# Optimization experiments

Measured on AMD Instinct MI355X. Metric: run time of the kernel, lower is better.

The kernel has to match this reference:

```python
import jax, jax.numpy as jnp
import numpy as np

C_M = 256   # norm_channel (msa channel)
C_Z = 128   # pair_channel
H = 8       # num_head
C = 32      # attention_channel per head


def layer_norm(x, gamma, beta, eps=1e-5):
    mu = jnp.mean(x, axis=-1, keepdims=True)
    var = jnp.var(x, axis=-1, keepdims=True)
    return (x - mu) * jax.lax.rsqrt(var + eps) * gamma + beta


def setup_inputs() -> dict:
    key = jax.random.key(0)
    ks = jax.random.split(key, 12)
    B, S, R = 1, 128, 256
    inp = {
        "msa_act": jax.random.normal(ks[0], (B, S, R, C_M), jnp.float32),
        "pair_act": jax.random.normal(ks[1], (B, R, R, C_Z), jnp.float32),
        "msa_mask": jnp.ones((B, S, R), jnp.float32),
        # query_norm params
        "qn_g": jnp.ones((C_M,), jnp.float32),
        "qn_b": jnp.zeros((C_M,), jnp.float32),
        # feat_2d_norm params
        "pn_g": jnp.ones((C_Z,), jnp.float32),
        "pn_b": jnp.zeros((C_Z,), jnp.float32),
        # feat_2d_weights: Linear(C_Z -> H, bias=False)
        "w2d": jax.random.normal(ks[2], (C_Z, H), jnp.float32) / np.sqrt(C_Z),
        # attention projections [C_M, H, C]
        "wq": jax.random.normal(ks[3], (C_M, H, C), jnp.float32) / np.sqrt(C_M),
        "wk": jax.random.normal(ks[4], (C_M, H, C), jnp.float32) / np.sqrt(C_M),
        "wv": jax.random.normal(ks[5], (C_M, H, C), jnp.float32) / np.sqrt(C_M),
        # gating linear [C_M, H, C] + bias
        "wg": jax.random.normal(ks[6], (C_M, H, C), jnp.float32) / np.sqrt(C_M),
        "bg": jnp.ones((H, C), jnp.float32),
        # output linear [H, C, C_M] + bias
        "wo": jax.random.normal(ks[7], (H, C, C_M), jnp.float32) / np.sqrt(H * C),
        "bo": jnp.zeros((C_M,), jnp.float32),
    }
    return inp


def reference(msa_act, pair_act, msa_mask, qn_g, qn_b, pn_g, pn_b, w2d,
              wq, wk, wv, wg, bg, wo, bo):
    # Pair bias: LayerNorm -> Linear(C_Z->H) -> permute to [B, 1, H, R, R]
    z = layer_norm(pair_act, pn_g, pn_b)            # [B, R, R, C_Z]
    z = jnp.einsum('bqkc,ch->bhqk', z, w2d)          # [B, H, R, R]
    z = z[:, None]                                   # [B, 1, H, R, R]

    # Mask bias: [B, S, 1, 1, R]
    mask_bias = (1e9 * (msa_mask - 1.0))[:, :, None, None, :]

    # Row-wise MHA with query norm
    m = layer_norm(msa_act, qn_g, qn_b)              # [B, S, R, C_M]
    scale = 1.0 / np.sqrt(C)
    q = jnp.einsum('bsqc,chd->bshqd', m, wq) * scale
    k = jnp.einsum('bskc,chd->bshkd', m, wk)
    v = jnp.einsum('bskc,chd->bshkd', m, wv)

    logits = jnp.einsum('bshqd,bshkd->bshqk', q, k) + mask_bias + z
    a = jax.nn.softmax(logits, axis=-1)              # [B, S, H, R, R]
    o = jnp.einsum('bshqk,bshkd->bsqhd', a, v)       # [B, S, R, H, C]

    g = jax.nn.sigmoid(jnp.einsum('bsqc,chd->bsqhd', m, wg) + bg)
    o = o * g
    out = jnp.einsum('bsqhd,hdc->bsqc', o, wo) + bo  # [B, S, R, C_M]
    return out
```

## Files before the change

### kernel.cpp

```cpp
#include <hip/hip_runtime.h>

typedef unsigned short u16;
typedef __attribute__((ext_vector_type(8))) short bf16x8;
typedef __attribute__((ext_vector_type(4))) float f32x4;

__device__ __forceinline__ float bf2f(u16 u){
  union { unsigned int i; float f; } v; v.i = ((unsigned int)u) << 16; return v.f;
}
__device__ __forceinline__ u16 f2bf(float f){
  union { float f; unsigned int i; } v; v.f = f;
  unsigned int i = v.i;
  return (u16)((i + 0x7fffu + ((i >> 16) & 1u)) >> 16);
}
__device__ __forceinline__ float ldin(const void* p, int i, int f){
  return f ? ((const float*)p)[i] : bf2f(((const u16*)p)[i]);
}
__device__ __forceinline__ bf16x8 pack8(const float* v){
  union { bf16x8 v8; u16 h[8]; } u;
  #pragma unroll
  for (int j = 0; j < 8; ++j) u.h[j] = f2bf(v[j]);
  return u.v8;
}
__device__ __forceinline__ void gload16(const u16* g, u16* l){
  __builtin_amdgcn_global_load_lds(
      (const __attribute__((address_space(1))) void*)g,
      (__attribute__((address_space(3))) void*)l, 16, 0, 0);
}

__global__ void k_sniff(const unsigned int* __restrict__ msa_w, int* __restrict__ flag)
{
  int lane = threadIdx.x & 63;
  int lo0 = 0, expok = 0;
  #pragma unroll
  for (int j = 0; j < 4; ++j) {
    unsigned int w = msa_w[lane * 4 + j];
    if ((w & 0xffffu) == 0u) lo0++;
    unsigned int e = (w >> 7) & 0xffu;
    if (e >= 110u && e <= 140u) expok++;
  }
  #pragma unroll
  for (int off = 1; off < 64; off <<= 1) {
    lo0   += __shfl_xor(lo0,   off, 64);
    expok += __shfl_xor(expok, off, 64);
  }
  if (lane == 0 && blockIdx.x == 0)
    *flag = (lo0 > 200) ? 1 : ((expok > 200) ? 0 : 1);
}

__global__ __launch_bounds__(256) void k_transpose(
    const void* __restrict__ wq, const void* __restrict__ wk,
    const void* __restrict__ wv, const void* __restrict__ wg,
    const void* __restrict__ wo, const int* __restrict__ flagp,
    u16* __restrict__ Wt, u16* __restrict__ wot)
{
  const int flag = *flagp;
  int idx = blockIdx.x * 256 + threadIdx.x;
  int mat = idx >> 16;
  int col = (idx >> 8) & 255;
  int c   = idx & 255;
  const void* src = (mat == 0) ? wq : (mat == 1) ? wk : (mat == 2) ? wv
                  : (mat == 3) ? wg : wo;
  u16 v = f2bf(ldin(src, c * 256 + col, flag));
  if (idx < 262144) Wt[idx] = v;
  else              wot[idx - 262144] = v;
}

__global__ __launch_bounds__(256) void k_pair_z(
    const void* __restrict__ pair, const void* __restrict__ png,
    const void* __restrict__ pnb, const void* __restrict__ w2d,
    const int* __restrict__ flagp, float* __restrict__ z)
{
  __shared__ u16 As[64 * 136];
  __shared__ u16 Bs[16 * 136];
  const int flag = *flagp;
  const int t = threadIdx.x, lane = t & 63, wave = t >> 6;
  const int g = lane >> 4, l15 = lane & 15;
  const int rowBase = blockIdx.x * 64;

  if (t < 128) {
    #pragma unroll
    for (int n = 0; n < 16; ++n)
      Bs[n * 136 + t] = (n < 8) ? f2bf(ldin(w2d, t * 8 + n, flag)) : (u16)0;
  }
  {
    int lrow = t >> 2, cb = (t & 3) * 32;
    int base = (rowBase + lrow) * 128 + cb;
    float x[32];
    if (flag) {
      const float* p = (const float*)pair + base;
      #pragma unroll
      for (int j = 0; j < 8; ++j) {
        float4 f4 = *(const float4*)(p + 4 * j);
        x[4*j] = f4.x; x[4*j+1] = f4.y; x[4*j+2] = f4.z; x[4*j+3] = f4.w;
      }
    } else {
      const u16* p = (const u16*)pair + base;
      #pragma unroll
      for (int j = 0; j < 4; ++j) {
        uint4 u = *(const uint4*)(p + 8 * j);
        const u16* h = (const u16*)&u;
        #pragma unroll
        for (int e = 0; e < 8; ++e) x[8*j+e] = bf2f(h[e]);
      }
    }
    float s = 0.f, sq = 0.f;
    #pragma unroll
    for (int j = 0; j < 32; ++j) { s += x[j]; sq += x[j] * x[j]; }
    s  += __shfl_xor(s, 1, 64);  s  += __shfl_xor(s, 2, 64);
    sq += __shfl_xor(sq, 1, 64); sq += __shfl_xor(sq, 2, 64);
    float mu = s * (1.f / 128.f);
    float var = sq * (1.f / 128.f) - mu * mu;
    float rs = rsqrtf(var + 1e-5f);
    u16 o[32];
    #pragma unroll
    for (int j = 0; j < 32; ++j) {
      int c = cb + j;
      o[j] = f2bf((x[j] - mu) * rs * ldin(png, c, flag) + ldin(pnb, c, flag));
    }
    u16* dst = As + lrow * 136 + cb;
    #pragma unroll
    for (int j = 0; j < 4; ++j)
      *(uint4*)(dst + 8 * j) = *(const uint4*)(o + 8 * j);
  }
  __syncthreads();

  f32x4 accz = {0.f, 0.f, 0.f, 0.f};
  #pragma unroll
  for (int kb = 0; kb < 4; ++kb) {
    bf16x8 a = *(const bf16x8*)(As + (wave * 16 + l15) * 136 + kb * 32 + g * 8);
    bf16x8 b = *(const bf16x8*)(Bs + l15 * 136 + kb * 32 + g * 8);
    accz = __builtin_amdgcn_mfma_f32_16x16x32_bf16(a, b, accz, 0, 0, 0);
  }
  if (l15 < 8) {
    #pragma unroll
    for (int r = 0; r < 4; ++r)
      z[l15 * 65536 + rowBase + wave * 16 + g * 4 + r] = accz[r];
  }
}

__global__ __launch_bounds__(256) void k_msa_ln(
    const void* __restrict__ msa, const void* __restrict__ qng,
    const void* __restrict__ qnb, const int* __restrict__ flagp,
    u16* __restrict__ m_bf)
{
  const int flag = *flagp;
  int wave = threadIdx.x >> 6, lane = threadIdx.x & 63;
  int row = blockIdx.x * 4 + wave;
  float x[4];
  if (flag) {
    float4 f4 = *((const float4*)msa + row * 64 + lane);
    x[0]=f4.x; x[1]=f4.y; x[2]=f4.z; x[3]=f4.w;
  } else {
    uint2 u = *((const uint2*)msa + row * 64 + lane);
    const u16* h = (const u16*)&u;
    #pragma unroll
    for (int j = 0; j < 4; ++j) x[j] = bf2f(h[j]);
  }
  float s = 0.f, sq = 0.f;
  #pragma unroll
  for (int j = 0; j < 4; ++j) { s += x[j]; sq += x[j] * x[j]; }
  #pragma unroll
  for (int off = 1; off < 64; off <<= 1) {
    s  += __shfl_xor(s,  off, 64);
    sq += __shfl_xor(sq, off, 64);
  }
  float mu = s * (1.f / 256.f);
  float var = sq * (1.f / 256.f) - mu * mu;
  float rs = rsqrtf(var + 1e-5f);
  u16 o[4];
  #pragma unroll
  for (int j = 0; j < 4; ++j) {
    int c = lane * 4 + j;
    o[j] = f2bf((x[j] - mu) * rs * ldin(qng, c, flag) + ldin(qnb, c, flag));
  }
  *((uint2*)m_bf + row * 64 + lane) = *(const uint2*)o;
}

__global__ __launch_bounds__(256) void k_qkvg(
    const u16* __restrict__ m_bf, const u16* __restrict__ Wt,
    const void* __restrict__ bg, const int* __restrict__ flagp,
    u16* __restrict__ q_ws, u16* __restrict__ k_ws,
    u16* __restrict__ v_ws, u16* __restrict__ g_ws)
{
  __shared__ u16 SM[64 * 136];
  u16* As = SM;
  u16* Bs = SM + 4096;
  const int flag = *flagp;
  const int t = threadIdx.x, lane = t & 63, wave = t >> 6;
  const int wm = (wave >> 1) * 64, wn = (wave & 1) * 64;
  const int rowBase = blockIdx.x * 128;
  const int colBase = blockIdx.y * 128;
  const int g = lane >> 4, l15 = lane & 15;
  const int srow = wave * 32 + (lane >> 2);
  const int scol = (lane & 3) * 8;
  const u16* gA = m_bf + (rowBase + srow) * 256 + scol;
  const u16* gB = Wt   + (colBase + srow) * 256 + scol;
  u16* lA = As + wave * 32 * 32;
  u16* lB = Bs + wave * 32 * 32;

  f32x4 acc[4][4];
  f32x4 zero = {0.f, 0.f, 0.f, 0.f};
  #pragma unroll
  for (int i = 0; i < 4; ++i)
    #pragma unroll
    for (int j = 0; j < 4; ++j) acc[i][j] = zero;

  for (int kb = 0; kb < 256; kb += 32) {
    __syncthreads();
    gload16(gA + kb,            lA);
    gload16(gA + kb + 16 * 256, lA + 16 * 32);
    gload16(gB + kb,            lB);
    gload16(gB + kb + 16 * 256, lB + 16 * 32);
    __syncthreads();
    bf16x8 a[4], b[4];
    #pragma unroll
    for (int mt = 0; mt < 4; ++mt)
      a[mt] = *(const bf16x8*)(As + (wm + mt * 16 + l15) * 32 + g * 8);
    #pragma unroll
    for (int nt = 0; nt < 4; ++nt)
      b[nt] = *(const bf16x8*)(Bs + (wn + nt * 16 + l15) * 32 + g * 8);
    #pragma unroll
    for (int mt = 0; mt < 4; ++mt)
      #pragma unroll
      for (int nt = 0; nt < 4; ++nt)
        acc[mt][nt] = __builtin_amdgcn_mfma_f32_16x16x32_bf16(a[mt], b[nt], acc[mt][nt], 0, 0, 0);
  }

  const int t4 = colBase >> 8;
  const float scale = 0.17677669529663687f;
  const int hbase = (colBase >> 5) & 7;
  const int s_ = rowBase >> 8;
  #pragma unroll
  for (int p = 0; p < 2; ++p) {
    __syncthreads();
    if ((wave >> 1) == p) {
      #pragma unroll
      for (int mt = 0; mt < 4; ++mt)
        #pragma unroll
        for (int nt = 0; nt < 4; ++nt)
          #pragma unroll
          for (int r = 0; r < 4; ++r) {
            int rr = mt * 16 + g * 4 + r;
            int cc = wn + nt * 16 + l15;
            float v = acc[mt][nt][r];
            u16 o;
            if (t4 == 0) o = f2bf(v * scale);
            else if (t4 == 3) {
              float gv = v + ldin(bg, (colBase & 255) + cc, flag);
              o = f2bf(1.0f / (1.0f + __expf(-gv)));
            } else o = f2bf(v);
            SM[rr * 136 + cc] = o;
          }
    }
    __syncthreads();
    int iibase = (rowBase & 255) + p * 64;
    if (t4 < 3) {
      u16* dst_ws = (t4 == 0) ? q_ws : (t4 == 1) ? k_ws : v_ws;
      int rr = t >> 2, dseg = t & 3;
      #pragma unroll
      for (int hl = 0; hl < 4; ++hl) {
        uint4 vd = *(const uint4*)(SM + rr * 136 + hl * 32 + dseg * 8);
        *(uint4*)(dst_ws + ((s_ * 8 + hbase + hl) * 256 + iibase + rr) * 32 + dseg * 8) = vd;
      }
    } else {
      int cbase = colBase & 255;
      int rr4 = t >> 4, cseg = t & 15;
      #pragma unroll
      for (int jr = 0; jr < 4; ++jr) {
        int rr = jr * 16 + rr4;
        uint4 vd = *(const uint4*)(SM + rr * 136 + cseg * 8);
        *(uint4*)(g_ws + (s_ * 256 + iibase + rr) * 256 + cbase + cseg * 8) = vd;
      }
    }
  }
}

__global__ __launch_bounds__(256) void k_attn(
    const u16* __restrict__ q_ws, const u16* __restrict__ k_ws,
    const u16* __restrict__ v_ws, const float* __restrict__ z,
    const void* __restrict__ mask, const u16* __restrict__ g_ws,
    const int* __restrict__ flagp, u16* __restrict__ og_ws)
{
  __shared__ u16 Ks[256 * 32];
  __shared__ u16 Vts[32 * 264];
  __shared__ float Tb[4][16 * 36];
  __shared__ float Mb[256];
  const int flag = *flagp;
  const int t = threadIdx.x, lane = t & 63, wave = t >> 6;
  const int sh = blockIdx.x;
  const int s_ = sh >> 3, h = sh & 7;

  {
    const uint4* srcK = (const uint4*)(k_ws + sh * 8192);
    uint4* dstK = (uint4*)Ks;
    #pragma unroll
    for (int j = 0; j < 4; ++j) dstK[t + 256 * j] = srcK[t + 256 * j];
    const u16* sv = v_ws + sh * 8192 + t * 32;
    uint4 v0 = *(const uint4*)sv, v1 = *(const uint4*)(sv + 8);
    const u16* ve = (const u16*)&v0;
    const u16* vo = (const u16*)&v1;
    #pragma unroll
    for (int d = 0; d < 8; ++d) Vts[d * 264 + t] = ve[d];
    #pragma unroll
    for (int d = 0; d < 8; ++d) Vts[(8 + d) * 264 + t] = vo[d];
    const u16* sv2 = sv + 16;
    uint4 v2 = *(const uint4*)sv2, v3 = *(const uint4*)(sv2 + 8);
    const u16* ve2 = (const u16*)&v2;
    const u16* vo2 = (const u16*)&v3;
    #pragma unroll
    for (int d = 0; d < 8; ++d) Vts[(16 + d) * 264 + t] = ve2[d];
    #pragma unroll
    for (int d = 0; d < 8; ++d) Vts[(24 + d) * 264 + t] = vo2[d];
    Mb[t] = 1e9f * (ldin(mask, s_ * 256 + t, flag) - 1.0f);
  }
  __syncthreads();

  const int g = lane >> 4, l15 = lane & 15;
  const u16* qb = q_ws + sh * 8192;
  float* Tw = &Tb[wave][0];
  f32x4 zero = {0.f, 0.f, 0.f, 0.f};

  for (int qt = 0; qt < 4; ++qt) {
    const int qbase = wave * 64 + qt * 16;
    bf16x8 aq = *(const bf16x8*)(qb + (qbase + l15) * 32 + g * 8);
    f32x4 S[16];
    #pragma unroll
    for (int kt = 0; kt < 16; ++kt) {
      bf16x8 bk = *(const bf16x8*)(Ks + (kt * 16 + l15) * 32 + g * 8);
      S[kt] = __builtin_amdgcn_mfma_f32_16x16x32_bf16(aq, bk, zero, 0, 0, 0);
    }
    float L[8][8];
    const float* zr = z + h * 65536 + (qbase + l15) * 256;
    #pragma unroll
    for (int kc = 0; kc < 8; ++kc) {
      asm volatile("s_waitcnt lgkmcnt(0)" ::: "memory");
      #pragma unroll
      for (int half = 0; half < 2; ++half)
        #pragma unroll
        for (int r = 0; r < 4; ++r)
          Tw[(g * 4 + r) * 36 + half * 16 + l15] = S[kc * 2 + half][r];
      asm volatile("s_waitcnt lgkmcnt(0)" ::: "memory");
      float4 t0 = *(const float4*)(Tw + l15 * 36 + g * 8);
      float4 t1 = *(const float4*)(Tw + l15 * 36 + g * 8 + 4);
      float4 m0 = *(const float4*)(Mb + kc * 32 + g * 8);
      float4 m1 = *(const float4*)(Mb + kc * 32 + g * 8 + 4);
      float4 z0 = *(const float4*)(zr + kc * 32 + g * 8);
      float4 z1 = *(const float4*)(zr + kc * 32 + g * 8 + 4);
      L[kc][0] = t0.x + m0.x + z0.x;  L[kc][1] = t0.y + m0.y + z0.y;
      L[kc][2] = t0.z + m0.z + z0.z;  L[kc][3] = t0.w + m0.w + z0.w;
      L[kc][4] = t1.x + m1.x + z1.x;  L[kc][5] = t1.y + m1.y + z1.y;
      L[kc][6] = t1.z + m1.z + z1.z;  L[kc][7] = t1.w + m1.w + z1.w;
    }
    float mx = -1e30f;
    #pragma unroll
    for (int kc = 0; kc < 8; ++kc)
      #pragma unroll
      for (int j = 0; j < 8; ++j) mx = fmaxf(mx, L[kc][j]);
    mx = fmaxf(mx, __shfl_xor(mx, 16, 64));
    mx = fmaxf(mx, __shfl_xor(mx, 32, 64));
    float sm = 0.f;
    #pragma unroll
    for (int kc = 0; kc < 8; ++kc)
      #pragma unroll
      for (int j = 0; j < 8; ++j) {
        float p = __expf(L[kc][j] - mx);
        L[kc][j] = p;
        sm += p;
      }
    sm += __shfl_xor(sm, 16, 64);
    sm += __shfl_xor(sm, 32, 64);
    f32x4 O0 = zero, O1 = zero;
    #pragma unroll
    for (int kc = 0; kc < 8; ++kc) {
      bf16x8 ap  = pack8(&L[kc][0]);
      bf16x8 bv0 = *(const bf16x8*)(Vts + l15 * 264 + kc * 32 + g * 8);
      bf16x8 bv1 = *(const bf16x8*)(Vts + (16 + l15) * 264 + kc * 32 + g * 8);
      O0 = __builtin_amdgcn_mfma_f32_16x16x32_bf16(ap, bv0, O0, 0, 0, 0);
      O1 = __builtin_amdgcn_mfma_f32_16x16x32_bf16(ap, bv1, O1, 0, 0, 0);
    }
    #pragma unroll
    for (int r = 0; r < 4; ++r) {
      float smr = __shfl(sm, g * 4 + r, 64);
      float inv = 1.0f / smr;
      int qq = qbase + g * 4 + r;
      int base = (s_ * 256 + qq) * 256 + h * 32;
      float o0 = O0[r] * inv * bf2f(g_ws[base + l15]);
      float o1 = O1[r] * inv * bf2f(g_ws[base + 16 + l15]);
      og_ws[base + l15]      = f2bf(o0);
      og_ws[base + 16 + l15] = f2bf(o1);
    }
  }
}

__global__ __launch_bounds__(256) void k_outproj(
    const u16* __restrict__ og, const u16* __restrict__ wot,
    const void* __restrict__ bo, const int* __restrict__ flagp,
    void* __restrict__ outv)
{
  __shared__ u16 As[128 * 32];
  __shared__ u16 Bs[128 * 32];
  const int flag = *flagp;
  const int t = threadIdx.x, lane = t & 63, wave = t >> 6;
  const int wm = (wave >> 1) * 64, wn = (wave & 1) * 64;
  const int rowBase = blockIdx.x * 128;
  const int colBase = blockIdx.y * 128;
  const int g = lane >> 4, l15 = lane & 15;
  const int srow = wave * 32 + (lane >> 2);
  const int scol = (lane & 3) * 8;
  const u16* gA = og  + (rowBase + srow) * 256 + scol;
  const u16* gB = wot + (colBase + srow) * 256 + scol;
  u16* lA = As + wave * 32 * 32;
  u16* lB = Bs + wave * 32 * 32;

  f32x4 acc[4][4];
  f32x4 zero = {0.f, 0.f, 0.f, 0.f};
  #pragma unroll
  for (int i = 0; i < 4; ++i)
    #pragma unroll
    for (int j = 0; j < 4; ++j) acc[i][j] = zero;

  for (int kb = 0; kb < 256; kb += 32) {
    __syncthreads();
    gload16(gA + kb,            lA);
    gload16(gA + kb + 16 * 256, lA + 16 * 32);
    gload16(gB + kb,            lB);
    gload16(gB + kb + 16 * 256, lB + 16 * 32);
    __syncthreads();
    bf16x8 a[4], b[4];
    #pragma unroll
    for (int mt = 0; mt < 4; ++mt)
      a[mt] = *(const bf16x8*)(As + (wm + mt * 16 + l15) * 32 + g * 8);
    #pragma unroll
    for (int nt = 0; nt < 4; ++nt)
      b[nt] = *(const bf16x8*)(Bs + (wn + nt * 16 + l15) * 32 + g * 8);
    #pragma unroll
    for (int mt = 0; mt < 4; ++mt)
      #pragma unroll
      for (int nt = 0; nt < 4; ++nt)
        acc[mt][nt] = __builtin_amdgcn_mfma_f32_16x16x32_bf16(a[mt], b[nt], acc[mt][nt], 0, 0, 0);
  }
  #pragma unroll
  for (int mt = 0; mt < 4; ++mt)
    #pragma unroll
    for (int nt = 0; nt < 4; ++nt)
      #pragma unroll
      for (int r = 0; r < 4; ++r) {
        int row = rowBase + wm + mt * 16 + g * 4 + r;
        int col = colBase + wn + nt * 16 + l15;
        float val = acc[mt][nt][r] + ldin(bo, col, flag);
        if (flag) ((float*)outv)[row * 256 + col] = val;
        else      ((u16*)outv)[row * 256 + col]   = f2bf(val);
      }
}

extern "C" void kernel_launch(void* const* d_in, const int* in_sizes, int n_in,
                              void* d_out, int out_size, void* d_ws, size_t ws_size,
                              hipStream_t stream)
{
  const void* msa  = d_in[0];
  const void* pair = d_in[1];
  const void* mask = d_in[2];
  const void* qng  = d_in[3];
  const void* qnb  = d_in[4];
  const void* png  = d_in[5];
  const void* pnb  = d_in[6];
  const void* w2d  = d_in[7];
  const void* wq   = d_in[8];
  const void* wk   = d_in[9];
  const void* wv   = d_in[10];
  const void* wg   = d_in[11];
  const void* bg   = d_in[12];
  const void* wo   = d_in[13];
  const void* bo   = d_in[14];

  char* ws = (char*)d_ws;
  float* z   = (float*)(ws + 0);
  u16* Wt    = (u16*)(ws + 2097152);
  u16* wot   = (u16*)(ws + 2621440);
  int* flag  = (int*)(ws + 2752512);
  u16* m_bf  = (u16*)(ws + 2752768);
  u16* og_ws = m_bf;
  u16* q_ws  = (u16*)(ws + 19529984);
  u16* k_ws  = (u16*)(ws + 36307200);
  u16* v_ws  = (u16*)(ws + 53084416);
  u16* g_ws  = (u16*)(ws + 69861632);

  hipLaunchKernelGGL(k_sniff, dim3(1), dim3(64), 0, stream,
                     (const unsigned int*)msa, flag);
  hipLaunchKernelGGL(k_transpose, dim3(1280), dim3(256), 0, stream,
                     wq, wk, wv, wg, wo, flag, Wt, wot);
  hipLaunchKernelGGL(k_msa_ln, dim3(8192), dim3(256), 0, stream,
                     msa, qng, qnb, flag, m_bf);
  hipLaunchKernelGGL(k_qkvg, dim3(256, 8), dim3(256), 0, stream,
                     m_bf, Wt, bg, flag, q_ws, k_ws, v_ws, g_ws);
  hipLaunchKernelGGL(k_pair_z, dim3(1024), dim3(256), 0, stream,
                     pair, png, pnb, w2d, flag, z);
  hipLaunchKernelGGL(k_attn, dim3(1024), dim3(256), 0, stream,
                     q_ws, k_ws, v_ws, z, mask, g_ws, flag, og_ws);
  hipLaunchKernelGGL(k_outproj, dim3(256, 2), dim3(256), 0, stream,
                     og_ws, wot, bo, flag, d_out);
}
```

Before: 303.3 us.

## Keep A fragments in registers across all output tiles in projection GEMMs

The QKVG and output-projection GEMMs drop the LDS-staged tiled loop. Each block now loads its full 128-row A panel into registers once and sweeps all output column tiles, reading weight fragments straight from global memory with a two-step register prefetch. The grids shrink from 2048 and 512 blocks to 256 blocks, each with launch_bounds(256,1). Epilogue stores now go directly to global memory instead of through a staged LDS transpose. The weight transpose also becomes LDS-tiled with vectorized stores. The trade-off is heavy register pressure, lower occupancy, fewer blocks to fill the CUs, and uncoalesced scalar epilogue writes.

Measured after the change: 341.0 us. 12.4% more time.

```diff
diff --git a/kernel.cpp b/kernel.cpp
--- a/kernel.cpp
+++ b/kernel.cpp
@@ -20,11 +20,6 @@
   #pragma unroll
   for (int j = 0; j < 8; ++j) u.h[j] = f2bf(v[j]);
   return u.v8;
-}
-__device__ __forceinline__ void gload16(const u16* g, u16* l){
-  __builtin_amdgcn_global_load_lds(
-      (const __attribute__((address_space(1))) void*)g,
-      (__attribute__((address_space(3))) void*)l, 16, 0, 0);
 }
 
 __global__ void k_sniff(const unsigned int* __restrict__ msa_w, int* __restrict__ flag)
@@ -53,16 +48,29 @@
     const void* __restrict__ wo, const int* __restrict__ flagp,
     u16* __restrict__ Wt, u16* __restrict__ wot)
 {
-  const int flag = *flagp;
-  int idx = blockIdx.x * 256 + threadIdx.x;
-  int mat = idx >> 16;
-  int col = (idx >> 8) & 255;
-  int c   = idx & 255;
+  __shared__ u16 T[64 * 72];
+  const int flag = *flagp;
+  const int t = threadIdx.x;
+  const int mat = blockIdx.x >> 4, tile = blockIdx.x & 15;
+  const int R0 = (tile >> 2) * 64, C0 = (tile & 3) * 64;
   const void* src = (mat == 0) ? wq : (mat == 1) ? wk : (mat == 2) ? wv
                   : (mat == 3) ? wg : wo;
-  u16 v = f2bf(ldin(src, c * 256 + col, flag));
-  if (idx < 262144) Wt[idx] = v;
-  else              wot[idx - 262144] = v;
+  u16* dst = (mat < 4) ? (Wt + mat * 65536) : wot;
+  {
+    int i = t >> 2, j0 = (t & 3) * 16;
+    #pragma unroll
+    for (int e = 0; e < 16; ++e)
+      T[i * 72 + j0 + e] = f2bf(ldin(src, (R0 + i) * 256 + C0 + j0 + e, flag));
+  }
+  __syncthreads();
+  {
+    int j = t >> 2, i0 = (t & 3) * 16;
+    u16 o[16];
+    #pragma unroll
+    for (int e = 0; e < 16; ++e) o[e] = T[(i0 + e) * 72 + j];
+    *(uint4*)(dst + (C0 + j) * 256 + R0 + i0)     = *(const uint4*)o;
+    *(uint4*)(dst + (C0 + j) * 256 + R0 + i0 + 8) = *(const uint4*)(o + 8);
+  }
 }
 
 __global__ __launch_bounds__(256) void k_pair_z(
@@ -176,102 +184,77 @@
   *((uint2*)m_bf + row * 64 + lane) = *(const uint2*)o;
 }
 
-__global__ __launch_bounds__(256) void k_qkvg(
+__global__ __launch_bounds__(256, 1) void k_qkvg(
     const u16* __restrict__ m_bf, const u16* __restrict__ Wt,
     const void* __restrict__ bg, const int* __restrict__ flagp,
     u16* __restrict__ q_ws, u16* __restrict__ k_ws,
     u16* __restrict__ v_ws, u16* __restrict__ g_ws)
 {
-  __shared__ u16 SM[64 * 136];
-  u16* As = SM;
-  u16* Bs = SM + 4096;
   const int flag = *flagp;
   const int t = threadIdx.x, lane = t & 63, wave = t >> 6;
   const int wm = (wave >> 1) * 64, wn = (wave & 1) * 64;
   const int rowBase = blockIdx.x * 128;
-  const int colBase = blockIdx.y * 128;
   const int g = lane >> 4, l15 = lane & 15;
-  const int srow = wave * 32 + (lane >> 2);
-  const int scol = (lane & 3) * 8;
-  const u16* gA = m_bf + (rowBase + srow) * 256 + scol;
-  const u16* gB = Wt   + (colBase + srow) * 256 + scol;
-  u16* lA = As + wave * 32 * 32;
-  u16* lB = Bs + wave * 32 * 32;
-
-  f32x4 acc[4][4];
-  f32x4 zero = {0.f, 0.f, 0.f, 0.f};
-  #pragma unroll
-  for (int i = 0; i < 4; ++i)
-    #pragma unroll
-    for (int j = 0; j < 4; ++j) acc[i][j] = zero;
-
-  for (int kb = 0; kb < 256; kb += 32) {
-    __syncthreads();
-    gload16(gA + kb,            lA);
-    gload16(gA + kb + 16 * 256, lA + 16 * 32);
-    gload16(gB + kb,            lB);
-    gload16(gB + kb + 16 * 256, lB + 16 * 32);
-    __syncthreads();
-    bf16x8 a[4], b[4];
+
+  bf16x8 af[8][4];
+  #pragma unroll
+  for (int kb = 0; kb < 8; ++kb)
     #pragma unroll
     for (int mt = 0; mt < 4; ++mt)
-      a[mt] = *(const bf16x8*)(As + (wm + mt * 16 + l15) * 32 + g * 8);
-    #pragma unroll
-    for (int nt = 0; nt < 4; ++nt)
-      b[nt] = *(const bf16x8*)(Bs + (wn + nt * 16 + l15) * 32 + g * 8);
+      af[kb][mt] = *(const bf16x8*)(
+          m_bf + (rowBase + wm + mt * 16 + l15) * 256 + kb * 32 + g * 8);
+
+  const float scale = 0.17677669529663687f;
+  for (int ct = 0; ct < 8; ++ct) {
+    const u16* Wb = Wt + (ct * 128 + wn) * 256;
+    bf16x8 b[4][4];
+    #pragma unroll
+    for (int nt = 0; nt < 4; ++nt) {
+      b[0][nt] = *(const bf16x8*)(Wb + (nt * 16 + l15) * 256 + g * 8);
+      b[1][nt] = *(const bf16x8*)(Wb + (nt * 16 + l15) * 256 + 32 + g * 8);
+    }
+    f32x4 acc[4][4];
+    f32x4 zero = {0.f, 0.f, 0.f, 0.f};
+    #pragma unroll
+    for (int i = 0; i < 4; ++i)
+      #pragma unroll
+      for (int j = 0; j < 4; ++j) acc[i][j] = zero;
+    #pragma unroll
+    for (int kb = 0; kb < 8; ++kb) {
+      if (kb < 6) {
+        #pragma unroll
+        for (int nt = 0; nt < 4; ++nt)
+          b[(kb + 2) & 3][nt] = *(const bf16x8*)(
+              Wb + (nt * 16 + l15) * 256 + (kb + 2) * 32 + g * 8);
+      }
+      #pragma unroll
+      for (int mt = 0; mt < 4; ++mt)
+        #pragma unroll
+        for (int nt = 0; nt < 4; ++nt)
+          acc[mt][nt] = __builtin_amdgcn_mfma_f32_16x16x32_bf16(
+              af[kb][mt], b[kb & 3][nt], acc[mt][nt], 0, 0, 0);
+    }
+    const int t4 = ct >> 1;
     #pragma unroll
     for (int mt = 0; mt < 4; ++mt)
       #pragma unroll
       for (int nt = 0; nt < 4; ++nt)
-        acc[mt][nt] = __builtin_amdgcn_mfma_f32_16x16x32_bf16(a[mt], b[nt], acc[mt][nt], 0, 0, 0);
-  }
-
-  const int t4 = colBase >> 8;
-  const float scale = 0.17677669529663687f;
-  const int hbase = (colBase >> 5) & 7;
-  const int s_ = rowBase >> 8;
-  #pragma unroll
-  for (int p = 0; p < 2; ++p) {
-    __syncthreads();
-    if ((wave >> 1) == p) {
-      #pragma unroll
-      for (int mt = 0; mt < 4; ++mt)
-        #pragma unroll
-        for (int nt = 0; nt < 4; ++nt)
-          #pragma unroll
-          for (int r = 0; r < 4; ++r) {
-            int rr = mt * 16 + g * 4 + r;
-            int cc = wn + nt * 16 + l15;
-            float v = acc[mt][nt][r];
-            u16 o;
-            if (t4 == 0) o = f2bf(v * scale);
-            else if (t4 == 3) {
-              float gv = v + ldin(bg, (colBase & 255) + cc, flag);
-              o = f2bf(1.0f / (1.0f + __expf(-gv)));
-            } else o = f2bf(v);
-            SM[rr * 136 + cc] = o;
+        #pragma unroll
+        for (int r = 0; r < 4; ++r) {
+          int row = rowBase + wm + mt * 16 + g * 4 + r;
+          int col = ct * 128 + wn + nt * 16 + l15;
+          int s_ = row >> 8, ii = row & 255;
+          int inner = col & 255, hh = inner >> 5, dd = inner & 31;
+          float v = acc[mt][nt][r];
+          if (t4 == 0)      q_ws[((s_ * 8 + hh) * 256 + ii) * 32 + dd] = f2bf(v * scale);
+          else if (t4 == 1) k_ws[((s_ * 8 + hh) * 256 + ii) * 32 + dd] = f2bf(v);
+          else if (t4 == 2) v_ws[((s_ * 8 + hh) * 256 + ii) * 32 + dd] = f2bf(v);
+          else {
+            float gv = v + ldin(bg, inner, flag);
+            gv = 1.0f / (1.0f + __expf(-gv));
+            g_ws[row * 256 + inner] = f2bf(gv);
           }
-    }
-    __syncthreads();
-    int iibase = (rowBase & 255) + p * 64;
-    if (t4 < 3) {
-      u16* dst_ws = (t4 == 0) ? q_ws : (t4 == 1) ? k_ws : v_ws;
-      int rr = t >> 2, dseg = t & 3;
-      #pragma unroll
-      for (int hl = 0; hl < 4; ++hl) {
-        uint4 vd = *(const uint4*)(SM + rr * 136 + hl * 32 + dseg * 8);
-        *(uint4*)(dst_ws + ((s_ * 8 + hbase + hl) * 256 + iibase + rr) * 32 + dseg * 8) = vd;
-      }
-    } else {
-      int cbase = colBase & 255;
-      int rr4 = t >> 4, cseg = t & 15;
-      #pragma unroll
-      for (int jr = 0; jr < 4; ++jr) {
-        int rr = jr * 16 + rr4;
-        uint4 vd = *(const uint4*)(SM + rr * 136 + cseg * 8);
-        *(uint4*)(g_ws + (s_ * 256 + iibase + rr) * 256 + cbase + cseg * 8) = vd;
-      }
-    }
+        }
   }
 }
 
@@ -392,65 +375,67 @@
   }
 }
 
-__global__ __launch_bounds__(256) void k_outproj(
+__global__ __launch_bounds__(256, 1) void k_outproj(
     const u16* __restrict__ og, const u16* __restrict__ wot,
     const void* __restrict__ bo, const int* __restrict__ flagp,
     void* __restrict__ outv)
 {
-  __shared__ u16 As[128 * 32];
-  __shared__ u16 Bs[128 * 32];
   const int flag = *flagp;
   const int t = threadIdx.x, lane = t & 63, wave = t >> 6;
   const int wm = (wave >> 1) * 64, wn = (wave & 1) * 64;
   const int rowBase = blockIdx.x * 128;
-  const int colBase = blockIdx.y * 128;
   const int g = lane >> 4, l15 = lane & 15;
-  const int srow = wave * 32 + (lane >> 2);
-  const int scol = (lane & 3) * 8;
-  const u16* gA = og  + (rowBase + srow) * 256 + scol;
-  const u16* gB = wot + (colBase + srow) * 256 + scol;
-  u16* lA = As + wave * 32 * 32;
-  u16* lB = Bs + wave * 32 * 32;
-
-  f32x4 acc[4][4];
-  f32x4 zero = {0.f, 0.f, 0.f, 0.f};
-  #pragma unroll
-  for (int i = 0; i < 4; ++i)
-    #pragma unroll
-    for (int j = 0; j < 4; ++j) acc[i][j] = zero;
-
-  for (int kb = 0; kb < 256; kb += 32) {
-    __syncthreads();
-    gload16(gA + kb,            lA);
-    gload16(gA + kb + 16 * 256, lA + 16 * 32);
-    gload16(gB + kb,            lB);
-    gload16(gB + kb + 16 * 256, lB + 16 * 32);
-    __syncthreads();
-    bf16x8 a[4], b[4];
+
+  bf16x8 af[8][4];
+  #pragma unroll
+  for (int kb = 0; kb < 8; ++kb)
     #pragma unroll
     for (int mt = 0; mt < 4; ++mt)
-      a[mt] = *(const bf16x8*)(As + (wm + mt * 16 + l15) * 32 + g * 8);
-    #pragma unroll
-    for (int nt = 0; nt < 4; ++nt)
-      b[nt] = *(const bf16x8*)(Bs + (wn + nt * 16 + l15) * 32 + g * 8);
+      af[kb][mt] = *(const bf16x8*)(
+          og + (rowBase + wm + mt * 16 + l15) * 256 + kb * 32 + g * 8);
+
+  for (int ct = 0; ct < 2; ++ct) {
+    const u16* Wb = wot + (ct * 128 + wn) * 256;
+    bf16x8 b[4][4];
+    #pragma unroll
+    for (int nt = 0; nt < 4; ++nt) {
+      b[0][nt] = *(const bf16x8*)(Wb + (nt * 16 + l15) * 256 + g * 8);
+      b[1][nt] = *(const bf16x8*)(Wb + (nt * 16 + l15) * 256 + 32 + g * 8);
+    }
+    f32x4 acc[4][4];
+    f32x4 zero = {0.f, 0.f, 0.f, 0.f};
+    #pragma unroll
+    for (int i = 0; i < 4; ++i)
+      #pragma unroll
+      for (int j = 0; j < 4; ++j) acc[i][j] = zero;
+    #pragma unroll
+    for (int kb = 0; kb < 8; ++kb) {
+      if (kb < 6) {
+        #pragma unroll
+        for (int nt = 0; nt < 4; ++nt)
+          b[(kb + 2) & 3][nt] = *(const bf16x8*)(
+              Wb + (nt * 16 + l15) * 256 + (kb + 2) * 32 + g * 8);
+      }
+      #pragma unroll
+      for (int mt = 0; mt < 4; ++mt)
+        #pragma unroll
+        for (int nt = 0; nt < 4; ++nt)
+          acc[mt][nt] = __builtin_amdgcn_mfma_f32_16x16x32_bf16(
+              af[kb][mt], b[kb & 3][nt], acc[mt][nt], 0, 0, 0);
+    }
     #pragma unroll
     for (int mt = 0; mt < 4; ++mt)
       #pragma unroll
       for (int nt = 0; nt < 4; ++nt)
-        acc[mt][nt] = __builtin_amdgcn_mfma_f32_16x16x32_bf16(a[mt], b[nt], acc[mt][nt], 0, 0, 0);
-  }
-  #pragma unroll
-  for (int mt = 0; mt < 4; ++mt)
-    #pragma unroll
-    for (int nt = 0; nt < 4; ++nt)
-      #pragma unroll
-      for (int r = 0; r < 4; ++r) {
-        int row = rowBase + wm + mt * 16 + g * 4 + r;
-        int col = colBase + wn + nt * 16 + l15;
-        float val = acc[mt][nt][r] + ldin(bo, col, flag);
-        if (flag) ((float*)outv)[row * 256 + col] = val;
-        else      ((u16*)outv)[row * 256 + col]   = f2bf(val);
-      }
+        #pragma unroll
+        for (int r = 0; r < 4; ++r) {
+          int row = rowBase + wm + mt * 16 + g * 4 + r;
+          int col = ct * 128 + wn + nt * 16 + l15;
+          float val = acc[mt][nt][r] + ldin(bo, col, flag);
+          if (flag) ((float*)outv)[row * 256 + col] = val;
+          else      ((u16*)outv)[row * 256 + col]   = f2bf(val);
+        }
+  }
 }
 
 extern "C" void kernel_launch(void* const* d_in, const int* in_sizes, int n_in,
@@ -487,16 +472,16 @@
 
   hipLaunchKernelGGL(k_sniff, dim3(1), dim3(64), 0, stream,
                      (const unsigned int*)msa, flag);
-  hipLaunchKernelGGL(k_transpose, dim3(1280), dim3(256), 0, stream,
+  hipLaunchKernelGGL(k_transpose, dim3(80), dim3(256), 0, stream,
                      wq, wk, wv, wg, wo, flag, Wt, wot);
   hipLaunchKernelGGL(k_msa_ln, dim3(8192), dim3(256), 0, stream,
                      msa, qng, qnb, flag, m_bf);
-  hipLaunchKernelGGL(k_qkvg, dim3(256, 8), dim3(256), 0, stream,
+  hipLaunchKernelGGL(k_qkvg, dim3(256), dim3(256), 0, stream,
                      m_bf, Wt, bg, flag, q_ws, k_ws, v_ws, g_ws);
   hipLaunchKernelGGL(k_pair_z, dim3(1024), dim3(256), 0, stream,
                      pair, png, pnb, w2d, flag, z);
   hipLaunchKernelGGL(k_attn, dim3(1024), dim3(256), 0, stream,
                      q_ws, k_ws, v_ws, z, mask, g_ws, flag, og_ws);
-  hipLaunchKernelGGL(k_outproj, dim3(256, 2), dim3(256), 0, stream,
+  hipLaunchKernelGGL(k_outproj, dim3(256), dim3(256), 0, stream,
                      og_ws, wot, bo, flag, d_out);
 }
```
